# Kernel optimization log

Measured on AMD Instinct MI355X. Metric: run time of the kernel, lower is better.

## Reference

```python
import jax, jax.numpy as jnp
import numpy as np

N = 20000   # nodes
E = 320000  # edges (before self-loops)
D = 256     # feature width (inChl = hdChl = outChl)
H = 4       # heads
C = D // H  # per-head channels = 64
NEG_SLOPE = 0.2
LN_EPS = 1e-5


def setup_inputs() -> dict:
    key = jax.random.key(0)
    ks = jax.random.split(key, 2 + 4 * 4)
    inp = {}
    inp["x"] = jax.random.normal(ks[0], (1, N, D), dtype=jnp.float32)
    inp["edge_index"] = jax.random.randint(ks[1], (2, E), 0, N, dtype=jnp.int32)
    s = 1.0 / np.sqrt(D)
    for i in range(4):
        k = 2 + 4 * i
        inp[f"Wl{i+1}"] = (jax.random.normal(ks[k], (D, H * C), dtype=jnp.float32) * s)
        inp[f"Wr{i+1}"] = (jax.random.normal(ks[k + 1], (D, H * C), dtype=jnp.float32) * s)
        inp[f"att{i+1}"] = (jax.random.normal(ks[k + 2], (H, C), dtype=jnp.float32) * s)
        inp[f"b{i+1}"] = jnp.zeros((H * C,), dtype=jnp.float32)
        inp[f"g{i+1}"] = jnp.ones((D,), dtype=jnp.float32)
        inp[f"be{i+1}"] = jnp.zeros((D,), dtype=jnp.float32)
    return inp


def _segment_softmax(scores, seg, num_segments):
    # scores: [E, H], per-destination softmax over incoming edges
    m = jax.ops.segment_max(scores, seg, num_segments=num_segments)
    e = jnp.exp(scores - m[seg])
    d = jax.ops.segment_sum(e, seg, num_segments=num_segments)
    return e / d[seg]


def _gatv2(x, src, dst, Wl, Wr, att, b):
    # GATv2Conv defaults: share_weights=False, concat=True, negative_slope=0.2
    n = x.shape[0]
    xl = (x @ Wl).reshape(n, H, C)  # source transform
    xr = (x @ Wr).reshape(n, H, C)  # target transform
    m = xl[src] + xr[dst]                                  # [E', H, C]
    e = jnp.sum(jax.nn.leaky_relu(m, NEG_SLOPE) * att, -1) # [E', H]
    alpha = _segment_softmax(e, dst, n)                    # [E', H]
    out = jax.ops.segment_sum(xl[src] * alpha[:, :, None], dst, num_segments=n)
    return out.reshape(n, H * C) + b


def _layernorm(x, g, b):
    mu = jnp.mean(x, -1, keepdims=True)
    var = jnp.mean(jnp.square(x - mu), -1, keepdims=True)
    return (x - mu) * jax.lax.rsqrt(var + LN_EPS) * g + b


def _forward(x, edge_index, layers):
    h = x[0]  # squeeze batch dim -> [N, D]
    n = h.shape[0]
    loop = jnp.arange(n, dtype=edge_index.dtype)
    src = jnp.concatenate([edge_index[0], loop])  # add_self_loops=True
    dst = jnp.concatenate([edge_index[1], loop])
    for (Wl, Wr, att, b, g, be) in layers:
        h = _gatv2(h, src, dst, Wl, Wr, att, b)
        h = jax.nn.relu(_layernorm(h, g, be))
    return h[None]  # unsqueeze -> [1, N, D]


def reference(x, edge_index,
              Wl1, Wr1, att1, b1, g1, be1,
              Wl2, Wr2, att2, b2, g2, be2,
              Wl3, Wr3, att3, b3, g3, be3,
              Wl4, Wr4, att4, b4, g4, be4):
    layers = [(Wl1, Wr1, att1, b1, g1, be1),
              (Wl2, Wr2, att2, b2, g2, be2),
              (Wl3, Wr3, att3, b3, g3, be3),
              (Wl4, Wr4, att4, b4, g4, be4)]
    return _forward(x, edge_index, layers)
```

## Files before the change

### kernel.cpp

```cpp
#include <hip/hip_runtime.h>
#include <math.h>

#define N_NODES 20000
#define E_EDGES 320000
#define EP (E_EDGES + N_NODES)
#define D 256
#define NHEAD 4
#define CH 64
#define NEG_SLOPE 0.2f
#define LN_EPS 1e-5f

typedef _Float16 half8_t __attribute__((ext_vector_type(8)));
typedef _Float16 half4_t __attribute__((ext_vector_type(4)));
typedef _Float16 half2_t __attribute__((ext_vector_type(2)));
typedef float   float4_t __attribute__((ext_vector_type(4)));

#define SCATTER_BLOCKS ((EP + 255) / 256)

__device__ __forceinline__ void async_cp16(const void* g, void* l)
{
    __builtin_amdgcn_global_load_lds(
        (const __attribute__((address_space(1))) void*)g,
        (__attribute__((address_space(3))) void*)l, 16, 0, 0);
}

template<int CTRL>
__device__ __forceinline__ float dpp_add(float v) {
    int t = __builtin_amdgcn_update_dpp(0, __float_as_int(v), CTRL, 0xF, 0xF, true);
    return v + __int_as_float(t);
}
__device__ __forceinline__ float row_sum16(float v) {
    v = dpp_add<0x121>(v);
    v = dpp_add<0x122>(v);
    v = dpp_add<0x124>(v);
    v = dpp_add<0x128>(v);
    return v;
}

__global__ __launch_bounds__(256)
void convert_hist_kernel(const float* __restrict__ x, _Float16* __restrict__ h16,
                         const int* __restrict__ ei, int* __restrict__ deg)
{
    int i = blockIdx.x * 256 + threadIdx.x;
    if (i < EP) {
        int dst = (i < E_EDGES) ? ei[E_EDGES + i] : (i - E_EDGES);
        atomicAdd(&deg[dst], 1);
    }
    if (i >= N_NODES * D / 4) return;
    float4 v = reinterpret_cast<const float4*>(x)[i];
    half4_t o;
    o.x = (_Float16)v.x; o.y = (_Float16)v.y; o.z = (_Float16)v.z; o.w = (_Float16)v.w;
    reinterpret_cast<half4_t*>(h16)[i] = o;
}

__global__ __launch_bounds__(1024)
void csr_scan_kernel(const int* __restrict__ deg, int* __restrict__ rowptr,
                     int* __restrict__ cursor, int* __restrict__ csr_src)
{
    __shared__ int buf[5120];
    __shared__ int wsum[16];
    __shared__ int carry_s;
    int t = threadIdx.x, lane = t & 63, w = t >> 6;
    if (t == 0) carry_s = 0;
    if (t < 8) csr_src[EP + t] = 0;

    for (int c = 0; c < 4; ++c) {
        int base = c * 5120;
        #pragma unroll
        for (int k = 0; k < 5; ++k) {
            int idx = base + k * 1024 + t;
            buf[k * 1024 + t] = (idx < N_NODES) ? deg[idx] : 0;
        }
        __syncthreads();
        int loc[5]; int s = 0;
        #pragma unroll
        for (int k = 0; k < 5; ++k) { loc[k] = buf[t * 5 + k]; s += loc[k]; }
        int x = s;
        #pragma unroll
        for (int o = 1; o < 64; o <<= 1) {
            int y = __shfl_up(x, o, 64);
            if (lane >= o) x += y;
        }
        if (lane == 63) wsum[w] = x;
        __syncthreads();
        if (t == 0) {
            int sa = carry_s;
            #pragma unroll
            for (int k = 0; k < 16; ++k) { int tmp = wsum[k]; wsum[k] = sa; sa += tmp; }
            carry_s = sa;
        }
        __syncthreads();
        int excl = wsum[w] + x - s;
        #pragma unroll
        for (int k = 0; k < 5; ++k) { buf[t * 5 + k] = excl; excl += loc[k]; }
        __syncthreads();
        #pragma unroll
        for (int k = 0; k < 5; ++k) {
            int idx = base + k * 1024 + t;
            if (idx < N_NODES) {
                int v = buf[k * 1024 + t];
                rowptr[idx] = v;
                cursor[idx] = v;
            }
        }
        __syncthreads();
    }
    if (t == 0) rowptr[N_NODES] = carry_s;
}

struct WPtrs { const float* p[8]; };
__global__ __launch_bounds__(256)
void scatter_convw_kernel(const int* __restrict__ ei, int* __restrict__ cursor,
                          int* __restrict__ csr_src, WPtrs wp,
                          _Float16* __restrict__ Wt_all)
{
    if (blockIdx.x < SCATTER_BLOCKS) {
        int e = blockIdx.x * 256 + threadIdx.x;
        if (e >= EP) return;
        int src, dst;
        if (e < E_EDGES) { src = ei[e]; dst = ei[E_EDGES + e]; }
        else             { src = dst = e - E_EDGES; }
        int pos = atomicAdd(&cursor[dst], 1);
        csr_src[pos] = src;
        return;
    }
    __shared__ float tile[64][65];
    int bz = blockIdx.x - SCATTER_BLOCKS;
    int bxi = bz & 3, byi = (bz >> 2) & 3, z = bz >> 4;
    const float* W = wp.p[z];
    _Float16* out = Wt_all + (size_t)z * 65536;
    int bx = bxi * 64, by = byi * 64;
    int t = threadIdx.x;
    #pragma unroll
    for (int i = 0; i < 16; ++i) {
        int idx = t + i * 256;
        int kk = idx >> 6, nn = idx & 63;
        tile[kk][nn] = W[(by + kk) * 256 + bx + nn];
    }
    __syncthreads();
    #pragma unroll
    for (int i = 0; i < 16; ++i) {
        int idx = t + i * 256;
        int nn = idx >> 6, kk = idx & 63;
        out[(bx + nn) * 256 + by + kk] = (_Float16)tile[kk][nn];
    }
}

#define BM 128
#define BN 128
#define BK 64
#define EPAD2 72
__global__ __launch_bounds__(256)
void gemm_f16_kernel(const _Float16* __restrict__ A16, const _Float16* __restrict__ Wt,
                     _Float16* __restrict__ X0, _Float16* __restrict__ X1, int nrows)
{
    const int b = blockIdx.x;
    const int pair = ((b >> 4) << 3) + (b & 7);
    const int z = (b >> 3) & 1;
    if (pair >= 314) return;
    const int yb = (pair >= 157) ? 1 : 0;
    const int xb = pair - yb * 157;

    const _Float16* W = Wt + z * 65536 + yb * (BN * 256);
    _Float16* X = z ? X1 : X0;
    const int row0 = xb * BM;
    const int col0 = yb * BN;

    __shared__ __align__(1024) char smem[BM * BK * 2 + BN * BK * 2];
    _Float16 (*As)[BK] = reinterpret_cast<_Float16 (*)[BK]>(smem);
    _Float16 (*Bs)[BK] = reinterpret_cast<_Float16 (*)[BK]>(smem + BM * BK * 2);
    _Float16* As_flat = reinterpret_cast<_Float16*>(smem);
    _Float16* Bs_flat = reinterpret_cast<_Float16*>(smem + BM * BK * 2);
    _Float16* ep = reinterpret_cast<_Float16*>(smem);

    const int tid  = threadIdx.x;
    const int wave = tid >> 6, lane = tid & 63;
    const int wy = wave >> 1, wx = wave & 1;
    const int quad = lane >> 4, l16 = lane & 15;

    float4_t acc[4][4];
    #pragma unroll
    for (int i = 0; i < 4; ++i)
        #pragma unroll
        for (int j = 0; j < 4; ++j) acc[i][j] = (float4_t)0.0f;

    const int r_in  = lane >> 3;
    const int c_in  = (lane & 7) * 8;

    #pragma unroll
    for (int k0 = 0; k0 < 256; k0 += BK) {
        #pragma unroll
        for (int j = 0; j < 4; ++j) {
            int ia  = wave * 4 + j;
            int row = ia * 8 + r_in;
            int gra = row0 + row;
            gra = (gra < nrows) ? gra : (nrows - 1);
            async_cp16(A16 + (size_t)gra * 256 + k0 + c_in, As_flat + ia * 512);
            async_cp16(W   + (size_t)row * 256 + k0 + c_in, Bs_flat + ia * 512);
        }
        __syncthreads();

        #pragma unroll
        for (int s = 0; s < 2; ++s) {
            half8_t af[4], bf[4];
            #pragma unroll
            for (int i = 0; i < 4; ++i)
                af[i] = *reinterpret_cast<const half8_t*>(&As[wy * 64 + i * 16 + l16][s * 32 + quad * 8]);
            #pragma unroll
            for (int j = 0; j < 4; ++j)
                bf[j] = *reinterpret_cast<const half8_t*>(&Bs[wx * 64 + j * 16 + l16][s * 32 + quad * 8]);
            #pragma unroll
            for (int i = 0; i < 4; ++i)
                #pragma unroll
                for (int j = 0; j < 4; ++j)
                    acc[i][j] = __builtin_amdgcn_mfma_f32_16x16x32_f16(af[i], bf[j], acc[i][j], 0, 0, 0);
        }
        __syncthreads();
    }

    _Float16* epw = ep + wave * 16 * EPAD2;
    #pragma unroll
    for (int it = 0; it < 4; ++it) {
        #pragma unroll
        for (int j = 0; j < 4; ++j)
            #pragma unroll
            for (int r = 0; r < 4; ++r)
                epw[(quad * 4 + r) * EPAD2 + j * 16 + l16] = (_Float16)acc[it][j][r];
        #pragma unroll
        for (int p = 0; p < 2; ++p) {
            int row = p * 8 + (lane >> 3);
            int col = (lane & 7) * 8;
            int gr = row0 + wy * 64 + it * 16 + row;
            half8_t v = *reinterpret_cast<const half8_t*>(&epw[row * EPAD2 + col]);
            if (gr < nrows)
                *reinterpret_cast<half8_t*>(X + gr * 256 + col0 + wx * 64 + col) = v;
        }
    }
}

__global__ __launch_bounds__(256)
void gat_fused_kernel(const _Float16* __restrict__ xl, const _Float16* __restrict__ xr,
                      const int* __restrict__ rowptr, const int* __restrict__ csr_src,
                      const float* __restrict__ att,
                      const float* __restrict__ bias, const float* __restrict__ g,
                      const float* __restrict__ be,
                      float* __restrict__ out32, _Float16* __restrict__ out16,
                      int write32)
{
    const int tid = threadIdx.x;
    const int w = tid >> 6, lane = tid & 63;
    const int n = blockIdx.x * 4 + w;
    const int start = rowptr[n], end = rowptr[n + 1];
    const int c0 = lane * 4;

    half2_t xr01, xr23, att01, att23;
    {
        half4_t xh = *reinterpret_cast<const half4_t*>(xr + n * D + c0);
        xr01.x = xh.x; xr01.y = xh.y; xr23.x = xh.z; xr23.y = xh.w;
        float4 av = *reinterpret_cast<const float4*>(att + c0);
        att01.x = (_Float16)av.x; att01.y = (_Float16)av.y;
        att23.x = (_Float16)av.z; att23.y = (_Float16)av.w;
    }
    const half2_t k02 = {(_Float16)NEG_SLOPE, (_Float16)NEG_SLOPE};

    float den = 0.0f;
    float4 num = make_float4(0.0f, 0.0f, 0.0f, 0.0f);

    int i = start;
    int nxt[8];
    if (i + 8 <= end) {
        #pragma unroll
        for (int j = 0; j < 8; ++j) nxt[j] = csr_src[i + j];
    }
    for (; i + 8 <= end; i += 8) {
        int sidx[8];
        #pragma unroll
        for (int j = 0; j < 8; ++j) sidx[j] = nxt[j];
        half4_t h[8];
        #pragma unroll
        for (int j = 0; j < 8; ++j)
            h[j] = *reinterpret_cast<const half4_t*>(xl + sidx[j] * D + c0);
        if (i + 16 <= end) {
            #pragma unroll
            for (int j = 0; j < 8; ++j) nxt[j] = csr_src[i + 8 + j];
        }
        float p[8];
        #pragma unroll
        for (int j = 0; j < 8; ++j) {
            half2_t a01 = {h[j].x, h[j].y}, a23 = {h[j].z, h[j].w};
            half2_t t0 = a01 + xr01, t1 = a23 + xr23;
            t0 = __builtin_elementwise_max(t0, t0 * k02);
            t1 = __builtin_elementwise_max(t1, t1 * k02);
            float v = __builtin_amdgcn_fdot2(t0, att01, 0.0f, false);
            p[j]    = __builtin_amdgcn_fdot2(t1, att23, v,   false);
        }
        #pragma unroll
        for (int j = 0; j < 8; ++j) p[j] = row_sum16(p[j]);
        #pragma unroll
        for (int j = 0; j < 8; ++j) p[j] = __expf(p[j]);
        #pragma unroll
        for (int j = 0; j < 8; ++j) {
            den += p[j];
            num.x = fmaf(p[j], (float)h[j].x, num.x);
            num.y = fmaf(p[j], (float)h[j].y, num.y);
            num.z = fmaf(p[j], (float)h[j].z, num.z);
            num.w = fmaf(p[j], (float)h[j].w, num.w);
        }
    }
    for (; i < end; i += 4) {
        int sidx[4];
        #pragma unroll
        for (int j = 0; j < 4; ++j) sidx[j] = csr_src[i + j];
        half4_t h[4];
        #pragma unroll
        for (int j = 0; j < 4; ++j)
            h[j] = *reinterpret_cast<const half4_t*>(xl + sidx[j] * D + c0);
        float p[4];
        #pragma unroll
        for (int j = 0; j < 4; ++j) {
            half2_t a01 = {h[j].x, h[j].y}, a23 = {h[j].z, h[j].w};
            half2_t t0 = a01 + xr01, t1 = a23 + xr23;
            t0 = __builtin_elementwise_max(t0, t0 * k02);
            t1 = __builtin_elementwise_max(t1, t1 * k02);
            float v = __builtin_amdgcn_fdot2(t0, att01, 0.0f, false);
            p[j]    = __builtin_amdgcn_fdot2(t1, att23, v,   false);
        }
        #pragma unroll
        for (int j = 0; j < 4; ++j) p[j] = row_sum16(p[j]);
        #pragma unroll
        for (int j = 0; j < 4; ++j) {
            float pj = (i + j < end) ? __expf(p[j]) : 0.0f;
            den += pj;
            num.x = fmaf(pj, (float)h[j].x, num.x);
            num.y = fmaf(pj, (float)h[j].y, num.y);
            num.z = fmaf(pj, (float)h[j].z, num.z);
            num.w = fmaf(pj, (float)h[j].w, num.w);
        }
    }

    float inv_den = 1.0f / den;
    float4 bi = *reinterpret_cast<const float4*>(bias + c0);
    float a0 = fmaf(num.x, inv_den, bi.x);
    float a1 = fmaf(num.y, inv_den, bi.y);
    float a2 = fmaf(num.z, inv_den, bi.z);
    float a3 = fmaf(num.w, inv_den, bi.w);

    float wsum = a0 + a1 + a2 + a3;
    float wsq  = a0 * a0 + a1 * a1 + a2 * a2 + a3 * a3;
    #pragma unroll
    for (int o = 1; o < 64; o <<= 1) {
        wsum += __shfl_xor(wsum, o, 64);
        wsq  += __shfl_xor(wsq,  o, 64);
    }
    float mu = wsum * (1.0f / 256.0f);
    float var = wsq * (1.0f / 256.0f) - mu * mu;
    float rstd = rsqrtf(var + LN_EPS);

    float4 gg = *reinterpret_cast<const float4*>(g + c0);
    float4 bb = *reinterpret_cast<const float4*>(be + c0);
    float o0 = fmaxf((a0 - mu) * rstd * gg.x + bb.x, 0.0f);
    float o1 = fmaxf((a1 - mu) * rstd * gg.y + bb.y, 0.0f);
    float o2 = fmaxf((a2 - mu) * rstd * gg.z + bb.z, 0.0f);
    float o3 = fmaxf((a3 - mu) * rstd * gg.w + bb.w, 0.0f);

    if (write32) {
        float4 o4 = make_float4(o0, o1, o2, o3);
        *reinterpret_cast<float4*>(out32 + n * D + c0) = o4;
    } else {
        half4_t o4;
        o4.x = (_Float16)o0; o4.y = (_Float16)o1; o4.z = (_Float16)o2; o4.w = (_Float16)o3;
        *reinterpret_cast<half4_t*>(out16 + n * D + c0) = o4;
    }
}

extern "C" void kernel_launch(void* const* d_in, const int* in_sizes, int n_in,
                              void* d_out, int out_size, void* d_ws, size_t ws_size,
                              hipStream_t stream)
{
    const float* x  = (const float*)d_in[0];
    const int*   ei = (const int*)d_in[1];

    char* ws = (char*)d_ws;
    size_t off = 0;
    _Float16* h16   = (_Float16*)(ws + off); off += (size_t)N_NODES * D * 2;
    _Float16* xl    = (_Float16*)(ws + off); off += (size_t)N_NODES * D * 2;
    _Float16* xr    = (_Float16*)(ws + off); off += (size_t)N_NODES * D * 2;
    _Float16* WtA   = (_Float16*)(ws + off); off += (size_t)8 * 65536 * 2;
    int* rowptr     = (int*)(ws + off);      off += (size_t)(N_NODES + 32) * 4;
    int* cursor     = (int*)(ws + off);      off += (size_t)N_NODES * 4;
    int* csr_src    = (int*)(ws + off);      off += (size_t)(EP + 32) * 4;

    WPtrs wp;
    for (int l = 0; l < 4; ++l) {
        wp.p[2 * l + 0] = (const float*)d_in[2 + 6 * l + 0];
        wp.p[2 * l + 1] = (const float*)d_in[2 + 6 * l + 1];
    }

    hipMemsetAsync(cursor, 0, (size_t)N_NODES * 4, stream);
    convert_hist_kernel<<<(N_NODES * D / 4 + 255) / 256, 256, 0, stream>>>(x, h16, ei, cursor);
    csr_scan_kernel<<<1, 1024, 0, stream>>>(cursor, rowptr, cursor, csr_src);
    scatter_convw_kernel<<<SCATTER_BLOCKS + 128, 256, 0, stream>>>(ei, cursor, csr_src, wp, WtA);

    for (int l = 0; l < 4; ++l) {
        const float* att  = (const float*)d_in[2 + 6 * l + 2];
        const float* bias = (const float*)d_in[2 + 6 * l + 3];
        const float* g    = (const float*)d_in[2 + 6 * l + 4];
        const float* be   = (const float*)d_in[2 + 6 * l + 5];

        gemm_f16_kernel<<<640, 256, 0, stream>>>(h16, WtA + (size_t)l * 131072,
                                                 xl, xr, N_NODES);
        gat_fused_kernel<<<N_NODES / 4, 256, 0, stream>>>(xl, xr, rowptr, csr_src, att,
                                                          bias, g, be,
                                                          (float*)d_out, h16, (l == 3) ? 1 : 0);
    }
}
```

Baseline: 329.8 us.

## Split wavefront into two half-waves processing alternate edge groups with 16-byte gathers

Each wavefront now splits into two 32-lane halves. Every lane owns 8 channels and loads a 16-byte half8 gather per edge, and the two halves walk disjoint groups of four edges in parallel. Source indices come in as int4 vector loads, the per-head reduction shrinks to an 8-lane DPP sum, and the two halves combine their partial numerator and denominator with a cross-half shuffle before LayerNorm. The aim is fewer, wider memory requests and half as many reduction steps per edge. In exchange it adds per-lane accumulator registers and a selection for the output store. The index loads can read past the end of each segment, and those reads are masked only in the tail.

```diff
diff --git a/kernel.cpp b/kernel.cpp
--- a/kernel.cpp
+++ b/kernel.cpp
@@ -14,6 +14,7 @@
 typedef _Float16 half4_t __attribute__((ext_vector_type(4)));
 typedef _Float16 half2_t __attribute__((ext_vector_type(2)));
 typedef float   float4_t __attribute__((ext_vector_type(4)));
+typedef int     iv4_t    __attribute__((ext_vector_type(4)));
 
 #define SCATTER_BLOCKS ((EP + 255) / 256)
 
@@ -29,12 +30,27 @@
     int t = __builtin_amdgcn_update_dpp(0, __float_as_int(v), CTRL, 0xF, 0xF, true);
     return v + __int_as_float(t);
 }
-__device__ __forceinline__ float row_sum16(float v) {
-    v = dpp_add<0x121>(v);
-    v = dpp_add<0x122>(v);
-    v = dpp_add<0x124>(v);
-    v = dpp_add<0x128>(v);
+__device__ __forceinline__ float grp8_sum(float v) {
+    v = dpp_add<0xB1>(v);
+    v = dpp_add<0x4E>(v);
+    v = dpp_add<0x141>(v);
     return v;
+}
+
+__device__ __forceinline__ iv4_t load_idx4(const int* p) {
+    iv4_t v;
+    __builtin_memcpy(&v, p, 16);
+    return v;
+}
+
+__device__ __forceinline__ float dot_att8(half8_t t, const half2_t a0, const half2_t a1,
+                                          const half2_t a2, const half2_t a3) {
+    half2_t t01 = {t[0], t[1]}, t23 = {t[2], t[3]};
+    half2_t t45 = {t[4], t[5]}, t67 = {t[6], t[7]};
+    float v = __builtin_amdgcn_fdot2(t01, a0, 0.0f, false);
+    v = __builtin_amdgcn_fdot2(t23, a1, v, false);
+    v = __builtin_amdgcn_fdot2(t45, a2, v, false);
+    return __builtin_amdgcn_fdot2(t67, a3, v, false);
 }
 
 __global__ __launch_bounds__(256)
@@ -250,105 +266,103 @@
     const int tid = threadIdx.x;
     const int w = tid >> 6, lane = tid & 63;
     const int n = blockIdx.x * 4 + w;
+    const int hs  = lane >> 5;
+    const int l32 = lane & 31;
+    const int c0  = l32 * 8;
     const int start = rowptr[n], end = rowptr[n + 1];
-    const int c0 = lane * 4;
-
-    half2_t xr01, xr23, att01, att23;
+
+    half8_t xrv = *reinterpret_cast<const half8_t*>(xr + (size_t)n * D + c0);
+    half2_t at0, at1, at2, at3;
     {
-        half4_t xh = *reinterpret_cast<const half4_t*>(xr + n * D + c0);
-        xr01.x = xh.x; xr01.y = xh.y; xr23.x = xh.z; xr23.y = xh.w;
-        float4 av = *reinterpret_cast<const float4*>(att + c0);
-        att01.x = (_Float16)av.x; att01.y = (_Float16)av.y;
-        att23.x = (_Float16)av.z; att23.y = (_Float16)av.w;
-    }
-    const half2_t k02 = {(_Float16)NEG_SLOPE, (_Float16)NEG_SLOPE};
+        float4 a0 = *reinterpret_cast<const float4*>(att + c0);
+        float4 a1 = *reinterpret_cast<const float4*>(att + c0 + 4);
+        at0 = half2_t{(_Float16)a0.x, (_Float16)a0.y};
+        at1 = half2_t{(_Float16)a0.z, (_Float16)a0.w};
+        at2 = half2_t{(_Float16)a1.x, (_Float16)a1.y};
+        at3 = half2_t{(_Float16)a1.z, (_Float16)a1.w};
+    }
+    const _Float16 slope = (_Float16)NEG_SLOPE;
 
     float den = 0.0f;
-    float4 num = make_float4(0.0f, 0.0f, 0.0f, 0.0f);
+    float num[8];
+    #pragma unroll
+    for (int k = 0; k < 8; ++k) num[k] = 0.0f;
 
     int i = start;
-    int nxt[8];
-    if (i + 8 <= end) {
-        #pragma unroll
-        for (int j = 0; j < 8; ++j) nxt[j] = csr_src[i + j];
-    }
+    iv4_t nxt = load_idx4(csr_src + i + 4 * hs);
     for (; i + 8 <= end; i += 8) {
-        int sidx[8];
-        #pragma unroll
-        for (int j = 0; j < 8; ++j) sidx[j] = nxt[j];
-        half4_t h[8];
-        #pragma unroll
-        for (int j = 0; j < 8; ++j)
-            h[j] = *reinterpret_cast<const half4_t*>(xl + sidx[j] * D + c0);
-        if (i + 16 <= end) {
-            #pragma unroll
-            for (int j = 0; j < 8; ++j) nxt[j] = csr_src[i + 8 + j];
-        }
-        float p[8];
-        #pragma unroll
-        for (int j = 0; j < 8; ++j) {
-            half2_t a01 = {h[j].x, h[j].y}, a23 = {h[j].z, h[j].w};
-            half2_t t0 = a01 + xr01, t1 = a23 + xr23;
-            t0 = __builtin_elementwise_max(t0, t0 * k02);
-            t1 = __builtin_elementwise_max(t1, t1 * k02);
-            float v = __builtin_amdgcn_fdot2(t0, att01, 0.0f, false);
-            p[j]    = __builtin_amdgcn_fdot2(t1, att23, v,   false);
-        }
-        #pragma unroll
-        for (int j = 0; j < 8; ++j) p[j] = row_sum16(p[j]);
-        #pragma unroll
-        for (int j = 0; j < 8; ++j) p[j] = __expf(p[j]);
-        #pragma unroll
-        for (int j = 0; j < 8; ++j) {
+        iv4_t cur = nxt;
+        half8_t h[4];
+        #pragma unroll
+        for (int j = 0; j < 4; ++j)
+            h[j] = *reinterpret_cast<const half8_t*>(xl + (size_t)cur[j] * D + c0);
+        nxt = load_idx4(csr_src + i + 8 + 4 * hs);
+        float p[4];
+        #pragma unroll
+        for (int j = 0; j < 4; ++j) {
+            half8_t t = h[j] + xrv;
+            t = __builtin_elementwise_max(t, t * slope);
+            p[j] = dot_att8(t, at0, at1, at2, at3);
+        }
+        #pragma unroll
+        for (int j = 0; j < 4; ++j) p[j] = grp8_sum(p[j]);
+        #pragma unroll
+        for (int j = 0; j < 4; ++j) p[j] = __expf(p[j]);
+        #pragma unroll
+        for (int j = 0; j < 4; ++j) {
             den += p[j];
-            num.x = fmaf(p[j], (float)h[j].x, num.x);
-            num.y = fmaf(p[j], (float)h[j].y, num.y);
-            num.z = fmaf(p[j], (float)h[j].z, num.z);
-            num.w = fmaf(p[j], (float)h[j].w, num.w);
-        }
-    }
-    for (; i < end; i += 4) {
-        int sidx[4];
-        #pragma unroll
-        for (int j = 0; j < 4; ++j) sidx[j] = csr_src[i + j];
-        half4_t h[4];
+            #pragma unroll
+            for (int k = 0; k < 8; ++k)
+                num[k] = fmaf(p[j], (float)h[j][k], num[k]);
+        }
+    }
+    if (i < end) {
+        iv4_t cur = nxt;
+        half8_t h[4];
         #pragma unroll
         for (int j = 0; j < 4; ++j)
-            h[j] = *reinterpret_cast<const half4_t*>(xl + sidx[j] * D + c0);
+            h[j] = *reinterpret_cast<const half8_t*>(xl + (size_t)cur[j] * D + c0);
         float p[4];
         #pragma unroll
         for (int j = 0; j < 4; ++j) {
-            half2_t a01 = {h[j].x, h[j].y}, a23 = {h[j].z, h[j].w};
-            half2_t t0 = a01 + xr01, t1 = a23 + xr23;
-            t0 = __builtin_elementwise_max(t0, t0 * k02);
-            t1 = __builtin_elementwise_max(t1, t1 * k02);
-            float v = __builtin_amdgcn_fdot2(t0, att01, 0.0f, false);
-            p[j]    = __builtin_amdgcn_fdot2(t1, att23, v,   false);
-        }
-        #pragma unroll
-        for (int j = 0; j < 4; ++j) p[j] = row_sum16(p[j]);
+            half8_t t = h[j] + xrv;
+            t = __builtin_elementwise_max(t, t * slope);
+            p[j] = dot_att8(t, at0, at1, at2, at3);
+        }
+        #pragma unroll
+        for (int j = 0; j < 4; ++j) p[j] = grp8_sum(p[j]);
         #pragma unroll
         for (int j = 0; j < 4; ++j) {
-            float pj = (i + j < end) ? __expf(p[j]) : 0.0f;
+            float pj = (i + 4 * hs + j < end) ? __expf(p[j]) : 0.0f;
             den += pj;
-            num.x = fmaf(pj, (float)h[j].x, num.x);
-            num.y = fmaf(pj, (float)h[j].y, num.y);
-            num.z = fmaf(pj, (float)h[j].z, num.z);
-            num.w = fmaf(pj, (float)h[j].w, num.w);
-        }
-    }
+            #pragma unroll
+            for (int k = 0; k < 8; ++k)
+                num[k] = fmaf(pj, (float)h[j][k], num[k]);
+        }
+    }
+
+    den += __shfl_xor(den, 32, 64);
+    #pragma unroll
+    for (int k = 0; k < 8; ++k) num[k] += __shfl_xor(num[k], 32, 64);
 
     float inv_den = 1.0f / den;
-    float4 bi = *reinterpret_cast<const float4*>(bias + c0);
-    float a0 = fmaf(num.x, inv_den, bi.x);
-    float a1 = fmaf(num.y, inv_den, bi.y);
-    float a2 = fmaf(num.z, inv_den, bi.z);
-    float a3 = fmaf(num.w, inv_den, bi.w);
-
-    float wsum = a0 + a1 + a2 + a3;
-    float wsq  = a0 * a0 + a1 * a1 + a2 * a2 + a3 * a3;
-    #pragma unroll
-    for (int o = 1; o < 64; o <<= 1) {
+    float4 b0 = *reinterpret_cast<const float4*>(bias + c0);
+    float4 b1 = *reinterpret_cast<const float4*>(bias + c0 + 4);
+    float a[8];
+    a[0] = fmaf(num[0], inv_den, b0.x);
+    a[1] = fmaf(num[1], inv_den, b0.y);
+    a[2] = fmaf(num[2], inv_den, b0.z);
+    a[3] = fmaf(num[3], inv_den, b0.w);
+    a[4] = fmaf(num[4], inv_den, b1.x);
+    a[5] = fmaf(num[5], inv_den, b1.y);
+    a[6] = fmaf(num[6], inv_den, b1.z);
+    a[7] = fmaf(num[7], inv_den, b1.w);
+
+    float wsum = 0.0f, wsq = 0.0f;
+    #pragma unroll
+    for (int k = 0; k < 8; ++k) { wsum += a[k]; wsq += a[k] * a[k]; }
+    #pragma unroll
+    for (int o = 1; o < 32; o <<= 1) {
         wsum += __shfl_xor(wsum, o, 64);
         wsq  += __shfl_xor(wsq,  o, 64);
     }
@@ -356,20 +370,31 @@
     float var = wsq * (1.0f / 256.0f) - mu * mu;
     float rstd = rsqrtf(var + LN_EPS);
 
-    float4 gg = *reinterpret_cast<const float4*>(g + c0);
-    float4 bb = *reinterpret_cast<const float4*>(be + c0);
-    float o0 = fmaxf((a0 - mu) * rstd * gg.x + bb.x, 0.0f);
-    float o1 = fmaxf((a1 - mu) * rstd * gg.y + bb.y, 0.0f);
-    float o2 = fmaxf((a2 - mu) * rstd * gg.z + bb.z, 0.0f);
-    float o3 = fmaxf((a3 - mu) * rstd * gg.w + bb.w, 0.0f);
-
+    float4 g0 = *reinterpret_cast<const float4*>(g + c0);
+    float4 g1 = *reinterpret_cast<const float4*>(g + c0 + 4);
+    float4 e0 = *reinterpret_cast<const float4*>(be + c0);
+    float4 e1 = *reinterpret_cast<const float4*>(be + c0 + 4);
+    float o8[8];
+    o8[0] = fmaxf((a[0] - mu) * rstd * g0.x + e0.x, 0.0f);
+    o8[1] = fmaxf((a[1] - mu) * rstd * g0.y + e0.y, 0.0f);
+    o8[2] = fmaxf((a[2] - mu) * rstd * g0.z + e0.z, 0.0f);
+    o8[3] = fmaxf((a[3] - mu) * rstd * g0.w + e0.w, 0.0f);
+    o8[4] = fmaxf((a[4] - mu) * rstd * g1.x + e1.x, 0.0f);
+    o8[5] = fmaxf((a[5] - mu) * rstd * g1.y + e1.y, 0.0f);
+    o8[6] = fmaxf((a[6] - mu) * rstd * g1.z + e1.z, 0.0f);
+    o8[7] = fmaxf((a[7] - mu) * rstd * g1.w + e1.w, 0.0f);
+
+    float s0 = hs ? o8[4] : o8[0];
+    float s1 = hs ? o8[5] : o8[1];
+    float s2 = hs ? o8[6] : o8[2];
+    float s3 = hs ? o8[7] : o8[3];
     if (write32) {
-        float4 o4 = make_float4(o0, o1, o2, o3);
-        *reinterpret_cast<float4*>(out32 + n * D + c0) = o4;
+        float4 ov = make_float4(s0, s1, s2, s3);
+        *reinterpret_cast<float4*>(out32 + (size_t)n * D + c0 + 4 * hs) = ov;
     } else {
-        half4_t o4;
-        o4.x = (_Float16)o0; o4.y = (_Float16)o1; o4.z = (_Float16)o2; o4.w = (_Float16)o3;
-        *reinterpret_cast<half4_t*>(out16 + n * D + c0) = o4;
+        half4_t ov;
+        ov.x = (_Float16)s0; ov.y = (_Float16)s1; ov.z = (_Float16)s2; ov.w = (_Float16)s3;
+        *reinterpret_cast<half4_t*>(out16 + (size_t)n * D + c0 + 4 * hs) = ov;
     }
 }
 
```

New measurement: 327.9 us, median of 2. No clear change (-0.6%).

## Split GAT aggregation per head with edge-parallel lanes and separate LayerNorm kernel

Applied to the files above, without the earlier changes.

The fused per-node aggregation kernel is replaced by a per-head kernel. Each wave handles one node and one head, with four 16-lane slots processing different edges at once, and the slot partial sums are then combined with cross-slot shuffles. LayerNorm and ReLU move to a separate kernel that reads an fp32 intermediate written into the output buffer. The intent is to raise parallelism and memory-level concurrency on the gather, at the cost of an extra launch, an fp32 round-trip of the node features, and four times as many blocks re-reading rowptr and csr_src.

```diff
diff --git a/kernel.cpp b/kernel.cpp
--- a/kernel.cpp
+++ b/kernel.cpp
@@ -29,11 +29,11 @@
     int t = __builtin_amdgcn_update_dpp(0, __float_as_int(v), CTRL, 0xF, 0xF, true);
     return v + __int_as_float(t);
 }
-__device__ __forceinline__ float row_sum16(float v) {
-    v = dpp_add<0x121>(v);
-    v = dpp_add<0x122>(v);
-    v = dpp_add<0x124>(v);
-    v = dpp_add<0x128>(v);
+__device__ __forceinline__ float grp16_sum(float v) {
+    v = dpp_add<0xB1>(v);
+    v = dpp_add<0x4E>(v);
+    v = dpp_add<0x141>(v);
+    v = dpp_add<0x140>(v);
     return v;
 }
 
@@ -62,7 +62,7 @@
     __shared__ int carry_s;
     int t = threadIdx.x, lane = t & 63, w = t >> 6;
     if (t == 0) carry_s = 0;
-    if (t < 8) csr_src[EP + t] = 0;
+    if (t < 16) csr_src[EP + t] = 0;
 
     for (int c = 0; c < 4; ++c) {
         int base = c * 5120;
@@ -239,114 +239,102 @@
 }
 
 __global__ __launch_bounds__(256)
-void gat_fused_kernel(const _Float16* __restrict__ xl, const _Float16* __restrict__ xr,
-                      const int* __restrict__ rowptr, const int* __restrict__ csr_src,
-                      const float* __restrict__ att,
-                      const float* __restrict__ bias, const float* __restrict__ g,
-                      const float* __restrict__ be,
-                      float* __restrict__ out32, _Float16* __restrict__ out16,
-                      int write32)
-{
-    const int tid = threadIdx.x;
-    const int w = tid >> 6, lane = tid & 63;
-    const int n = blockIdx.x * 4 + w;
+void gat_head_kernel(const _Float16* __restrict__ xl, const _Float16* __restrict__ xr,
+                     const int* __restrict__ rowptr, const int* __restrict__ csr_src,
+                     const float* __restrict__ att, const float* __restrict__ bias,
+                     float* __restrict__ hout)
+{
+    const int bid = blockIdx.x;
+    const int h   = bid & 3;
+    const int grp = bid >> 2;
+    const int wave = threadIdx.x >> 6, lane = threadIdx.x & 63;
+    const int n = grp * 4 + wave;
+    const int slot = lane >> 4, l16 = lane & 15;
+    const int C0 = h * 64 + l16 * 4;
     const int start = rowptr[n], end = rowptr[n + 1];
+
+    half4_t xrv = *reinterpret_cast<const half4_t*>(xr + (size_t)n * D + C0);
+    half2_t at01, at23;
+    {
+        float4 av = *reinterpret_cast<const float4*>(att + C0);
+        at01 = half2_t{(_Float16)av.x, (_Float16)av.y};
+        at23 = half2_t{(_Float16)av.z, (_Float16)av.w};
+    }
+    const _Float16 slope = (_Float16)NEG_SLOPE;
+
+    float den = 0.0f;
+    float num0 = 0.0f, num1 = 0.0f, num2 = 0.0f, num3 = 0.0f;
+
+    int i = start;
+    int nxa = csr_src[i + slot];
+    int nxb = csr_src[i + 4 + slot];
+    for (; i + 8 <= end; i += 8) {
+        int ca = nxa, cb = nxb;
+        half4_t ha = *reinterpret_cast<const half4_t*>(xl + (size_t)ca * D + C0);
+        half4_t hb = *reinterpret_cast<const half4_t*>(xl + (size_t)cb * D + C0);
+        nxa = csr_src[i + 8 + slot];
+        nxb = csr_src[i + 12 + slot];
+        half4_t ta = ha + xrv; ta = __builtin_elementwise_max(ta, ta * slope);
+        half4_t tb = hb + xrv; tb = __builtin_elementwise_max(tb, tb * slope);
+        float pa = __builtin_amdgcn_fdot2(half2_t{ta.x, ta.y}, at01, 0.0f, false);
+        pa = __builtin_amdgcn_fdot2(half2_t{ta.z, ta.w}, at23, pa, false);
+        float pb = __builtin_amdgcn_fdot2(half2_t{tb.x, tb.y}, at01, 0.0f, false);
+        pb = __builtin_amdgcn_fdot2(half2_t{tb.z, tb.w}, at23, pb, false);
+        pa = grp16_sum(pa); pb = grp16_sum(pb);
+        pa = __expf(pa);    pb = __expf(pb);
+        den += pa + pb;
+        num0 = fmaf(pa, (float)ha.x, num0); num0 = fmaf(pb, (float)hb.x, num0);
+        num1 = fmaf(pa, (float)ha.y, num1); num1 = fmaf(pb, (float)hb.y, num1);
+        num2 = fmaf(pa, (float)ha.z, num2); num2 = fmaf(pb, (float)hb.z, num2);
+        num3 = fmaf(pa, (float)ha.w, num3); num3 = fmaf(pb, (float)hb.w, num3);
+    }
+    if (i < end) {
+        int ca = nxa, cb = nxb;
+        half4_t ha = *reinterpret_cast<const half4_t*>(xl + (size_t)ca * D + C0);
+        half4_t hb = *reinterpret_cast<const half4_t*>(xl + (size_t)cb * D + C0);
+        half4_t ta = ha + xrv; ta = __builtin_elementwise_max(ta, ta * slope);
+        half4_t tb = hb + xrv; tb = __builtin_elementwise_max(tb, tb * slope);
+        float pa = __builtin_amdgcn_fdot2(half2_t{ta.x, ta.y}, at01, 0.0f, false);
+        pa = __builtin_amdgcn_fdot2(half2_t{ta.z, ta.w}, at23, pa, false);
+        float pb = __builtin_amdgcn_fdot2(half2_t{tb.x, tb.y}, at01, 0.0f, false);
+        pb = __builtin_amdgcn_fdot2(half2_t{tb.z, tb.w}, at23, pb, false);
+        pa = grp16_sum(pa); pb = grp16_sum(pb);
+        pa = (i + slot < end)     ? __expf(pa) : 0.0f;
+        pb = (i + 4 + slot < end) ? __expf(pb) : 0.0f;
+        den += pa + pb;
+        num0 = fmaf(pa, (float)ha.x, num0); num0 = fmaf(pb, (float)hb.x, num0);
+        num1 = fmaf(pa, (float)ha.y, num1); num1 = fmaf(pb, (float)hb.y, num1);
+        num2 = fmaf(pa, (float)ha.z, num2); num2 = fmaf(pb, (float)hb.z, num2);
+        num3 = fmaf(pa, (float)ha.w, num3); num3 = fmaf(pb, (float)hb.w, num3);
+    }
+
+    den  += __shfl_xor(den,  16, 64); den  += __shfl_xor(den,  32, 64);
+    num0 += __shfl_xor(num0, 16, 64); num0 += __shfl_xor(num0, 32, 64);
+    num1 += __shfl_xor(num1, 16, 64); num1 += __shfl_xor(num1, 32, 64);
+    num2 += __shfl_xor(num2, 16, 64); num2 += __shfl_xor(num2, 32, 64);
+    num3 += __shfl_xor(num3, 16, 64); num3 += __shfl_xor(num3, 32, 64);
+
+    if (slot == 0) {
+        float inv = 1.0f / den;
+        float4 bi = *reinterpret_cast<const float4*>(bias + C0);
+        float4 o = make_float4(fmaf(num0, inv, bi.x), fmaf(num1, inv, bi.y),
+                               fmaf(num2, inv, bi.z), fmaf(num3, inv, bi.w));
+        *reinterpret_cast<float4*>(hout + (size_t)n * D + C0) = o;
+    }
+}
+
+__global__ __launch_bounds__(256)
+void ln_relu_kernel(const float* __restrict__ hin, const float* __restrict__ g,
+                    const float* __restrict__ be, _Float16* __restrict__ out16,
+                    float* __restrict__ out32, int write32)
+{
+    const int wave = threadIdx.x >> 6, lane = threadIdx.x & 63;
+    const int n = blockIdx.x * 4 + wave;
     const int c0 = lane * 4;
-
-    half2_t xr01, xr23, att01, att23;
-    {
-        half4_t xh = *reinterpret_cast<const half4_t*>(xr + n * D + c0);
-        xr01.x = xh.x; xr01.y = xh.y; xr23.x = xh.z; xr23.y = xh.w;
-        float4 av = *reinterpret_cast<const float4*>(att + c0);
-        att01.x = (_Float16)av.x; att01.y = (_Float16)av.y;
-        att23.x = (_Float16)av.z; att23.y = (_Float16)av.w;
-    }
-    const half2_t k02 = {(_Float16)NEG_SLOPE, (_Float16)NEG_SLOPE};
-
-    float den = 0.0f;
-    float4 num = make_float4(0.0f, 0.0f, 0.0f, 0.0f);
-
-    int i = start;
-    int nxt[8];
-    if (i + 8 <= end) {
-        #pragma unroll
-        for (int j = 0; j < 8; ++j) nxt[j] = csr_src[i + j];
-    }
-    for (; i + 8 <= end; i += 8) {
-        int sidx[8];
-        #pragma unroll
-        for (int j = 0; j < 8; ++j) sidx[j] = nxt[j];
-        half4_t h[8];
-        #pragma unroll
-        for (int j = 0; j < 8; ++j)
-            h[j] = *reinterpret_cast<const half4_t*>(xl + sidx[j] * D + c0);
-        if (i + 16 <= end) {
-            #pragma unroll
-            for (int j = 0; j < 8; ++j) nxt[j] = csr_src[i + 8 + j];
-        }
-        float p[8];
-        #pragma unroll
-        for (int j = 0; j < 8; ++j) {
-            half2_t a01 = {h[j].x, h[j].y}, a23 = {h[j].z, h[j].w};
-            half2_t t0 = a01 + xr01, t1 = a23 + xr23;
-            t0 = __builtin_elementwise_max(t0, t0 * k02);
-            t1 = __builtin_elementwise_max(t1, t1 * k02);
-            float v = __builtin_amdgcn_fdot2(t0, att01, 0.0f, false);
-            p[j]    = __builtin_amdgcn_fdot2(t1, att23, v,   false);
-        }
-        #pragma unroll
-        for (int j = 0; j < 8; ++j) p[j] = row_sum16(p[j]);
-        #pragma unroll
-        for (int j = 0; j < 8; ++j) p[j] = __expf(p[j]);
-        #pragma unroll
-        for (int j = 0; j < 8; ++j) {
-            den += p[j];
-            num.x = fmaf(p[j], (float)h[j].x, num.x);
-            num.y = fmaf(p[j], (float)h[j].y, num.y);
-            num.z = fmaf(p[j], (float)h[j].z, num.z);
-            num.w = fmaf(p[j], (float)h[j].w, num.w);
-        }
-    }
-    for (; i < end; i += 4) {
-        int sidx[4];
-        #pragma unroll
-        for (int j = 0; j < 4; ++j) sidx[j] = csr_src[i + j];
-        half4_t h[4];
-        #pragma unroll
-        for (int j = 0; j < 4; ++j)
-            h[j] = *reinterpret_cast<const half4_t*>(xl + sidx[j] * D + c0);
-        float p[4];
-        #pragma unroll
-        for (int j = 0; j < 4; ++j) {
-            half2_t a01 = {h[j].x, h[j].y}, a23 = {h[j].z, h[j].w};
-            half2_t t0 = a01 + xr01, t1 = a23 + xr23;
-            t0 = __builtin_elementwise_max(t0, t0 * k02);
-            t1 = __builtin_elementwise_max(t1, t1 * k02);
-            float v = __builtin_amdgcn_fdot2(t0, att01, 0.0f, false);
-            p[j]    = __builtin_amdgcn_fdot2(t1, att23, v,   false);
-        }
-        #pragma unroll
-        for (int j = 0; j < 4; ++j) p[j] = row_sum16(p[j]);
-        #pragma unroll
-        for (int j = 0; j < 4; ++j) {
-            float pj = (i + j < end) ? __expf(p[j]) : 0.0f;
-            den += pj;
-            num.x = fmaf(pj, (float)h[j].x, num.x);
-            num.y = fmaf(pj, (float)h[j].y, num.y);
-            num.z = fmaf(pj, (float)h[j].z, num.z);
-            num.w = fmaf(pj, (float)h[j].w, num.w);
-        }
-    }
-
-    float inv_den = 1.0f / den;
-    float4 bi = *reinterpret_cast<const float4*>(bias + c0);
-    float a0 = fmaf(num.x, inv_den, bi.x);
-    float a1 = fmaf(num.y, inv_den, bi.y);
-    float a2 = fmaf(num.z, inv_den, bi.z);
-    float a3 = fmaf(num.w, inv_den, bi.w);
-
-    float wsum = a0 + a1 + a2 + a3;
-    float wsq  = a0 * a0 + a1 * a1 + a2 * a2 + a3 * a3;
+    float4 a = *reinterpret_cast<const float4*>(hin + (size_t)n * D + c0);
+
+    float wsum = a.x + a.y + a.z + a.w;
+    float wsq  = a.x * a.x + a.y * a.y + a.z * a.z + a.w * a.w;
     #pragma unroll
     for (int o = 1; o < 64; o <<= 1) {
         wsum += __shfl_xor(wsum, o, 64);
@@ -358,18 +346,17 @@
 
     float4 gg = *reinterpret_cast<const float4*>(g + c0);
     float4 bb = *reinterpret_cast<const float4*>(be + c0);
-    float o0 = fmaxf((a0 - mu) * rstd * gg.x + bb.x, 0.0f);
-    float o1 = fmaxf((a1 - mu) * rstd * gg.y + bb.y, 0.0f);
-    float o2 = fmaxf((a2 - mu) * rstd * gg.z + bb.z, 0.0f);
-    float o3 = fmaxf((a3 - mu) * rstd * gg.w + bb.w, 0.0f);
+    float o0 = fmaxf((a.x - mu) * rstd * gg.x + bb.x, 0.0f);
+    float o1 = fmaxf((a.y - mu) * rstd * gg.y + bb.y, 0.0f);
+    float o2 = fmaxf((a.z - mu) * rstd * gg.z + bb.z, 0.0f);
+    float o3 = fmaxf((a.w - mu) * rstd * gg.w + bb.w, 0.0f);
 
     if (write32) {
-        float4 o4 = make_float4(o0, o1, o2, o3);
-        *reinterpret_cast<float4*>(out32 + n * D + c0) = o4;
+        *reinterpret_cast<float4*>(out32 + (size_t)n * D + c0) = make_float4(o0, o1, o2, o3);
     } else {
-        half4_t o4;
-        o4.x = (_Float16)o0; o4.y = (_Float16)o1; o4.z = (_Float16)o2; o4.w = (_Float16)o3;
-        *reinterpret_cast<half4_t*>(out16 + n * D + c0) = o4;
+        half4_t ov;
+        ov.x = (_Float16)o0; ov.y = (_Float16)o1; ov.z = (_Float16)o2; ov.w = (_Float16)o3;
+        *reinterpret_cast<half4_t*>(out16 + (size_t)n * D + c0) = ov;
     }
 }
 
@@ -390,6 +377,8 @@
     int* cursor     = (int*)(ws + off);      off += (size_t)N_NODES * 4;
     int* csr_src    = (int*)(ws + off);      off += (size_t)(EP + 32) * 4;
 
+    float* hout = (float*)d_out;
+
     WPtrs wp;
     for (int l = 0; l < 4; ++l) {
         wp.p[2 * l + 0] = (const float*)d_in[2 + 6 * l + 0];
@@ -409,8 +398,9 @@
 
         gemm_f16_kernel<<<640, 256, 0, stream>>>(h16, WtA + (size_t)l * 131072,
                                                  xl, xr, N_NODES);
-        gat_fused_kernel<<<N_NODES / 4, 256, 0, stream>>>(xl, xr, rowptr, csr_src, att,
-                                                          bias, g, be,
-                                                          (float*)d_out, h16, (l == 3) ? 1 : 0);
-    }
-}
+        gat_head_kernel<<<N_NODES, 256, 0, stream>>>(xl, xr, rowptr, csr_src,
+                                                     att, bias, hout);
+        ln_relu_kernel<<<N_NODES / 4, 256, 0, stream>>>(hout, g, be, h16,
+                                                        hout, (l == 3) ? 1 : 0);
+    }
+}
```

Result: slower. 369.0 us (+11.9%).
